# Performance work log

Measured on AMD Instinct MI355X. Metric: run time of the kernel, lower is better.

The kernel has to match this reference:

```python
import jax, jax.numpy as jnp
import numpy as np

IN_F, OUT_F = 128, 128
B, N = 4, 4096

def setup_inputs() -> dict:
    key = jax.random.key(0)
    k1, k2, k3 = jax.random.split(key, 3)
    relation_matrix = jax.random.uniform(k1, (B, N, N), dtype=jnp.float32)
    inputs = jax.random.normal(k2, (B, N, IN_F), dtype=jnp.float32)
    w = jax.random.normal(k3, (IN_F, OUT_F), dtype=jnp.float32)
    return {"relation_matrix": relation_matrix, "inputs": inputs, "w": w}

def reference(relation_matrix, inputs, w):
    # deg_i = sum_j A_ij ; D = diag(deg) + I  -> inverse is elementwise reciprocal
    deg = jnp.sum(relation_matrix, axis=-1) + 1.0            # [B, N]
    # (A + I) @ X  == A @ X + X  (avoids materializing A + eye)
    ax = jnp.einsum('bnm,bmf->bnf', relation_matrix, inputs) + inputs  # [B, N, in]
    z = (ax / deg[..., None]) @ w                            # [B, N, out]
    return jax.nn.relu(z)
```

## Files before the change

### kernel.cpp

```cpp
#include <hip/hip_runtime.h>
#include <hip/hip_bf16.h>
#include <stdint.h>

#define NN 4096
#define NF 128
#define NB 4
#define KC 128
#define NSTAGE (NN / KC)

typedef __attribute__((ext_vector_type(4))) float  floatx4;
typedef __attribute__((ext_vector_type(8))) __bf16 bf16x8;

__device__ __forceinline__ void load_lds_16(const float* g, float* l) {
    __builtin_amdgcn_global_load_lds(
        (const __attribute__((address_space(1))) uint32_t*)g,
        (__attribute__((address_space(3))) uint32_t*)l, 16, 0, 0);
}

__global__ __launch_bounds__(256) void prep_kernel(const float* __restrict__ X,
                                                   const float* __restrict__ w,
                                                   __bf16* __restrict__ Xpack,
                                                   __bf16* __restrict__ wpack) {
    __shared__ float Xs[32][129];
    const int tid = threadIdx.x;
    const int bx  = blockIdx.x;
    if (bx == 512) {
        for (int p = tid; p < 512; p += 256) {
            int kc = p >> 7, n = p & 127;
#pragma unroll
            for (int k8 = 0; k8 < 32; k8 += 8) {
                bf16x8 v;
#pragma unroll
                for (int j = 0; j < 8; j++)
                    v[j] = (__bf16)w[(size_t)(kc * 32 + k8 + j) * NF + n];
                *(bf16x8*)(wpack + ((size_t)(kc * 128 + n)) * 32 + k8) = v;
            }
        }
        return;
    }
    const int b  = bx >> 7;
    const int kc = bx & 127;
    const float* Xt = X + ((size_t)b * NN + (size_t)kc * 32) * NF;
#pragma unroll
    for (int j = 0; j < 16; j++) {
        int i = tid + j * 256;
        Xs[i >> 7][i & 127] = Xt[i];
    }
    __syncthreads();
    const int f  = tid >> 1;
    const int kh = (tid & 1) * 16;
    bf16x8 v0, v1;
#pragma unroll
    for (int j = 0; j < 8; j++) v0[j] = (__bf16)Xs[kh + j][f];
#pragma unroll
    for (int j = 0; j < 8; j++) v1[j] = (__bf16)Xs[kh + 8 + j][f];
    __bf16* op = Xpack + (((size_t)b * 128 + kc) * 128 + f) * 32 + kh;
    *(bf16x8*)op = v0;
    *(bf16x8*)(op + 8) = v1;
}

__global__ __launch_bounds__(512, 2) void main_kernel(const float* __restrict__ A,
                                                      const float* __restrict__ X,
                                                      const __bf16* __restrict__ Xpack,
                                                      const __bf16* __restrict__ wpack,
                                                      float* __restrict__ out) {
    __shared__ float  At[2][32][260];
    __shared__ __bf16 Us[64][136];

    const int tid  = threadIdx.x;
    const int wv   = tid >> 6;
    const int lane = tid & 63;
    const int lm   = lane & 15;
    const int quad = lane >> 4;
    const int rg   = wv & 1;
    const int cg   = wv >> 1;

    const int b  = blockIdx.x >> 6;
    const int m0 = (blockIdx.x & 63) << 6;

    const float* Asrc = A + ((size_t)b * NN + m0 + (lane >> 5)) * NN + (lane & 31) * 4;

    const __bf16* Bbase = Xpack + ((size_t)b * 128 * NF + (cg * 32 + lm)) * 32 + quad * 8;

    floatx4 acc[2][2];
#pragma unroll
    for (int i = 0; i < 2; i++)
#pragma unroll
        for (int j = 0; j < 2; j++) acc[i][j] = (floatx4){0.f, 0.f, 0.f, 0.f};
    float ds0 = 0.f, ds1 = 0.f;

#pragma unroll
    for (int j = 0; j < 4; j++)
        load_lds_16(Asrc + (size_t)(wv * 4 + j) * 2 * NN, &At[0][wv * 4 + j][0]);

    const int r0 = rg * 32 + lm;
    const int r1 = r0 + 16;
    const int ofs0 = (r0 & 1) * 128 + quad * 8;
    const int ofs1 = (r1 & 1) * 128 + quad * 8;

    for (int s = 0; s < NSTAGE; s++) {
        const int buf = s & 1;
        __builtin_amdgcn_s_waitcnt(0x0f70);
        __syncthreads();
        if (s + 1 < NSTAGE) {
#pragma unroll
            for (int j = 0; j < 4; j++)
                load_lds_16(Asrc + (size_t)(wv * 4 + j) * 2 * NN + (size_t)(s + 1) * KC,
                            &At[buf ^ 1][wv * 4 + j][0]);
        }
        const float(*Ab)[260] = At[buf];
        const __bf16* Bs = Bbase + (size_t)s * 4 * 4096;
#pragma unroll
        for (int kk = 0; kk < 4; kk++) {
            bf16x8 b0 = *(const bf16x8*)(Bs + (size_t)kk * 4096);
            bf16x8 b1 = *(const bf16x8*)(Bs + (size_t)kk * 4096 + 512);
            floatx4 a00 = *(const floatx4*)&Ab[r0 >> 1][ofs0 + kk * 32];
            floatx4 a01 = *(const floatx4*)&Ab[r0 >> 1][ofs0 + kk * 32 + 4];
            floatx4 a10 = *(const floatx4*)&Ab[r1 >> 1][ofs1 + kk * 32];
            floatx4 a11 = *(const floatx4*)&Ab[r1 >> 1][ofs1 + kk * 32 + 4];
            ds0 += a00[0] + a00[1] + a00[2] + a00[3] + a01[0] + a01[1] + a01[2] + a01[3];
            ds1 += a10[0] + a10[1] + a10[2] + a10[3] + a11[0] + a11[1] + a11[2] + a11[3];
            bf16x8 af0, af1;
#pragma unroll
            for (int i = 0; i < 4; i++) { af0[i] = (__bf16)a00[i]; af0[4 + i] = (__bf16)a01[i]; }
#pragma unroll
            for (int i = 0; i < 4; i++) { af1[i] = (__bf16)a10[i]; af1[4 + i] = (__bf16)a11[i]; }
            acc[0][0] = __builtin_amdgcn_mfma_f32_16x16x32_bf16(af0, b0, acc[0][0], 0, 0, 0);
            acc[0][1] = __builtin_amdgcn_mfma_f32_16x16x32_bf16(af0, b1, acc[0][1], 0, 0, 0);
            acc[1][0] = __builtin_amdgcn_mfma_f32_16x16x32_bf16(af1, b0, acc[1][0], 0, 0, 0);
            acc[1][1] = __builtin_amdgcn_mfma_f32_16x16x32_bf16(af1, b1, acc[1][1], 0, 0, 0);
        }
    }

    ds0 += __shfl_xor(ds0, 16, 64); ds0 += __shfl_xor(ds0, 32, 64);
    ds1 += __shfl_xor(ds1, 16, 64); ds1 += __shfl_xor(ds1, 32, 64);
    float deg0[4], deg1[4];
#pragma unroll
    for (int i = 0; i < 4; i++) {
        deg0[i] = __shfl(ds0, quad * 4 + i, 64) + 1.0f;
        deg1[i] = __shfl(ds1, quad * 4 + i, 64) + 1.0f;
    }

    bf16x8 wf[4][2];
#pragma unroll
    for (int kc2 = 0; kc2 < 4; kc2++)
#pragma unroll
        for (int nt = 0; nt < 2; nt++)
            wf[kc2][nt] = *(const bf16x8*)(wpack +
                ((size_t)(kc2 * 128 + cg * 32 + nt * 16 + lm)) * 32 + quad * 8);

    const float* Xb = X + ((size_t)b * NN + m0) * NF;
#pragma unroll
    for (int sub = 0; sub < 2; sub++) {
#pragma unroll
        for (int nt = 0; nt < 2; nt++) {
            int col = cg * 32 + nt * 16 + lm;
#pragma unroll
            for (int i = 0; i < 4; i++) {
                int r = rg * 32 + sub * 16 + quad * 4 + i;
                float d = sub ? deg1[i] : deg0[i];
                float u = (acc[sub][nt][i] + Xb[(size_t)r * NF + col]) / d;
                Us[r][col] = (__bf16)u;
            }
        }
    }
    __syncthreads();

    float* ob = out + ((size_t)b * NN + m0) * NF;
#pragma unroll
    for (int sub = 0; sub < 2; sub++) {
        int rm = rg * 32 + sub * 16;
        floatx4 z0 = {0.f, 0.f, 0.f, 0.f};
        floatx4 z1 = {0.f, 0.f, 0.f, 0.f};
#pragma unroll
        for (int kc2 = 0; kc2 < 4; kc2++) {
            bf16x8 ua = *(const bf16x8*)&Us[rm + lm][kc2 * 32 + quad * 8];
            z0 = __builtin_amdgcn_mfma_f32_16x16x32_bf16(ua, wf[kc2][0], z0, 0, 0, 0);
            z1 = __builtin_amdgcn_mfma_f32_16x16x32_bf16(ua, wf[kc2][1], z1, 0, 0, 0);
        }
#pragma unroll
        for (int nt = 0; nt < 2; nt++) {
            int col = cg * 32 + nt * 16 + lm;
            floatx4 zv = nt ? z1 : z0;
#pragma unroll
            for (int i = 0; i < 4; i++) {
                int r = rm + quad * 4 + i;
                float v = zv[i];
                ob[(size_t)r * NF + col] = v > 0.f ? v : 0.f;
            }
        }
    }
}

extern "C" void kernel_launch(void* const* d_in, const int* in_sizes, int n_in,
                              void* d_out, int out_size, void* d_ws, size_t ws_size,
                              hipStream_t stream) {
    const float* A = (const float*)d_in[0];
    const float* X = (const float*)d_in[1];
    const float* w = (const float*)d_in[2];
    float* out = (float*)d_out;

    __bf16* Xpack = (__bf16*)d_ws;
    __bf16* wpack = Xpack + (size_t)NB * NF * NN;

    prep_kernel<<<513, 256, 0, stream>>>(X, w, Xpack, wpack);
    main_kernel<<<256, 512, 0, stream>>>(A, X, Xpack, wpack, out);
}
```

Baseline: 390.1 us.

## Triple-buffer A tiles with smaller K-chunks and prefetch distance two

Halves the K chunk to 64 and replaces the double-buffered LDS ring with a three-stage ring, so A loads run two stages ahead and the vmcnt wait only blocks on the older stage. The Xpack B fragments are loaded before the next prefetch is issued, with sched_barriers pinning the order, and the Us epilogue buffer now aliases the A ring to save LDS, which needs an extra barrier. The smaller chunks double the number of barriers per block, and the aliasing relies on the final barrier ordering being correct.

```diff
diff --git a/kernel.cpp b/kernel.cpp
--- a/kernel.cpp
+++ b/kernel.cpp
@@ -5,7 +5,7 @@
 #define NN 4096
 #define NF 128
 #define NB 4
-#define KC 128
+#define KC 64
 #define NSTAGE (NN / KC)
 
 typedef __attribute__((ext_vector_type(4))) float  floatx4;
@@ -64,8 +64,8 @@
                                                       const __bf16* __restrict__ Xpack,
                                                       const __bf16* __restrict__ wpack,
                                                       float* __restrict__ out) {
-    __shared__ float  At[2][32][260];
-    __shared__ __bf16 Us[64][136];
+    __shared__ float At[3][16][260];
+    __bf16(*Us)[136] = (__bf16(*)[136]) & At[0][0][0];
 
     const int tid  = threadIdx.x;
     const int wv   = tid >> 6;
@@ -78,7 +78,11 @@
     const int b  = blockIdx.x >> 6;
     const int m0 = (blockIdx.x & 63) << 6;
 
-    const float* Asrc = A + ((size_t)b * NN + m0 + (lane >> 5)) * NN + (lane & 31) * 4;
+    const float* Asrc[2];
+#pragma unroll
+    for (int j = 0; j < 2; j++)
+        Asrc[j] = A + ((size_t)b * NN + m0 + 4 * (wv * 2 + j) + (lane >> 4)) * NN
+                    + (lane & 15) * 4;
 
     const __bf16* Bbase = Xpack + ((size_t)b * 128 * NF + (cg * 32 + lm)) * 32 + quad * 8;
 
@@ -89,35 +93,43 @@
         for (int j = 0; j < 2; j++) acc[i][j] = (floatx4){0.f, 0.f, 0.f, 0.f};
     float ds0 = 0.f, ds1 = 0.f;
 
-#pragma unroll
-    for (int j = 0; j < 4; j++)
-        load_lds_16(Asrc + (size_t)(wv * 4 + j) * 2 * NN, &At[0][wv * 4 + j][0]);
-
     const int r0 = rg * 32 + lm;
     const int r1 = r0 + 16;
-    const int ofs0 = (r0 & 1) * 128 + quad * 8;
-    const int ofs1 = (r1 & 1) * 128 + quad * 8;
-
-    for (int s = 0; s < NSTAGE; s++) {
-        const int buf = s & 1;
-        __builtin_amdgcn_s_waitcnt(0x0f70);
-        __syncthreads();
-        if (s + 1 < NSTAGE) {
-#pragma unroll
-            for (int j = 0; j < 4; j++)
-                load_lds_16(Asrc + (size_t)(wv * 4 + j) * 2 * NN + (size_t)(s + 1) * KC,
-                            &At[buf ^ 1][wv * 4 + j][0]);
-        }
-        const float(*Ab)[260] = At[buf];
-        const __bf16* Bs = Bbase + (size_t)s * 4 * 4096;
-#pragma unroll
-        for (int kk = 0; kk < 4; kk++) {
-            bf16x8 b0 = *(const bf16x8*)(Bs + (size_t)kk * 4096);
-            bf16x8 b1 = *(const bf16x8*)(Bs + (size_t)kk * 4096 + 512);
-            floatx4 a00 = *(const floatx4*)&Ab[r0 >> 1][ofs0 + kk * 32];
-            floatx4 a01 = *(const floatx4*)&Ab[r0 >> 1][ofs0 + kk * 32 + 4];
-            floatx4 a10 = *(const floatx4*)&Ab[r1 >> 1][ofs1 + kk * 32];
-            floatx4 a11 = *(const floatx4*)&Ab[r1 >> 1][ofs1 + kk * 32 + 4];
+    const int c0 = r0 >> 2, o0 = (r0 & 3) * 64 + quad * 8;
+    const int c1 = r1 >> 2, o1 = (r1 & 3) * 64 + quad * 8;
+
+#pragma unroll
+    for (int j = 0; j < 2; j++) load_lds_16(Asrc[j], &At[0][wv * 2 + j][0]);
+#pragma unroll
+    for (int j = 0; j < 2; j++) load_lds_16(Asrc[j] + KC, &At[1][wv * 2 + j][0]);
+
+    auto stage = [&](int s, bool last) {
+        if (last) __builtin_amdgcn_s_waitcnt(0x0f70);
+        else      __builtin_amdgcn_s_waitcnt(0x0f72);
+        __builtin_amdgcn_s_barrier();
+        __builtin_amdgcn_sched_barrier(0);
+        const int buf = s % 3;
+        bf16x8 bfr[2][2];
+        const __bf16* Bs = Bbase + (size_t)(2 * s) * 4096;
+#pragma unroll
+        for (int kk = 0; kk < 2; kk++) {
+            bfr[kk][0] = *(const bf16x8*)(Bs + (size_t)kk * 4096);
+            bfr[kk][1] = *(const bf16x8*)(Bs + (size_t)kk * 4096 + 512);
+        }
+        __builtin_amdgcn_sched_barrier(0);
+        if (s + 2 < NSTAGE) {
+            const int wbuf = (s + 2) % 3;
+#pragma unroll
+            for (int j = 0; j < 2; j++)
+                load_lds_16(Asrc[j] + (size_t)(s + 2) * KC, &At[wbuf][wv * 2 + j][0]);
+        }
+        __builtin_amdgcn_sched_barrier(0);
+#pragma unroll
+        for (int kk = 0; kk < 2; kk++) {
+            floatx4 a00 = *(const floatx4*)&At[buf][c0][o0 + kk * 32];
+            floatx4 a01 = *(const floatx4*)&At[buf][c0][o0 + kk * 32 + 4];
+            floatx4 a10 = *(const floatx4*)&At[buf][c1][o1 + kk * 32];
+            floatx4 a11 = *(const floatx4*)&At[buf][c1][o1 + kk * 32 + 4];
             ds0 += a00[0] + a00[1] + a00[2] + a00[3] + a01[0] + a01[1] + a01[2] + a01[3];
             ds1 += a10[0] + a10[1] + a10[2] + a10[3] + a11[0] + a11[1] + a11[2] + a11[3];
             bf16x8 af0, af1;
@@ -125,12 +137,15 @@
             for (int i = 0; i < 4; i++) { af0[i] = (__bf16)a00[i]; af0[4 + i] = (__bf16)a01[i]; }
 #pragma unroll
             for (int i = 0; i < 4; i++) { af1[i] = (__bf16)a10[i]; af1[4 + i] = (__bf16)a11[i]; }
-            acc[0][0] = __builtin_amdgcn_mfma_f32_16x16x32_bf16(af0, b0, acc[0][0], 0, 0, 0);
-            acc[0][1] = __builtin_amdgcn_mfma_f32_16x16x32_bf16(af0, b1, acc[0][1], 0, 0, 0);
-            acc[1][0] = __builtin_amdgcn_mfma_f32_16x16x32_bf16(af1, b0, acc[1][0], 0, 0, 0);
-            acc[1][1] = __builtin_amdgcn_mfma_f32_16x16x32_bf16(af1, b1, acc[1][1], 0, 0, 0);
-        }
-    }
+            acc[0][0] = __builtin_amdgcn_mfma_f32_16x16x32_bf16(af0, bfr[kk][0], acc[0][0], 0, 0, 0);
+            acc[0][1] = __builtin_amdgcn_mfma_f32_16x16x32_bf16(af0, bfr[kk][1], acc[0][1], 0, 0, 0);
+            acc[1][0] = __builtin_amdgcn_mfma_f32_16x16x32_bf16(af1, bfr[kk][0], acc[1][0], 0, 0, 0);
+            acc[1][1] = __builtin_amdgcn_mfma_f32_16x16x32_bf16(af1, bfr[kk][1], acc[1][1], 0, 0, 0);
+        }
+    };
+
+    for (int s = 0; s < NSTAGE - 1; s++) stage(s, false);
+    stage(NSTAGE - 1, true);
 
     ds0 += __shfl_xor(ds0, 16, 64); ds0 += __shfl_xor(ds0, 32, 64);
     ds1 += __shfl_xor(ds1, 16, 64); ds1 += __shfl_xor(ds1, 32, 64);
@@ -148,6 +163,8 @@
         for (int nt = 0; nt < 2; nt++)
             wf[kc2][nt] = *(const bf16x8*)(wpack +
                 ((size_t)(kc2 * 128 + cg * 32 + nt * 16 + lm)) * 32 + quad * 8);
+
+    __syncthreads();
 
     const float* Xb = X + ((size_t)b * NN + m0) * NF;
 #pragma unroll
```

Result: slower. 407.3 us (+4.4%).
